# Kernel tuning notes

Measured on AMD Instinct MI355X. Metric: run time of the kernel, lower is better.

Reference implementation:

```python
import jax, jax.numpy as jnp
import numpy as np

S, B, D_IN, D_H, D_OUT = 32, 1024, 784, 1024, 10


def setup_inputs() -> dict:
    key = jax.random.key(0)
    ks = jax.random.split(key, 8)
    inp = {
        "x": jax.random.normal(ks[0], (B, D_IN), dtype=jnp.float32),
        # variational means / log-variances (init like the torch module)
        "wm0": jax.random.normal(ks[1], (D_IN, D_H), dtype=jnp.float32) * 0.1,
        "wv0": jnp.full((D_IN, D_H), -6.0, dtype=jnp.float32),
        "bm0": jnp.full((D_H,), 0.1, dtype=jnp.float32),
        "bv0": jnp.full((D_H,), -6.0, dtype=jnp.float32),
        "wm1": jax.random.normal(ks[2], (D_H, D_H), dtype=jnp.float32) * 0.1,
        "wv1": jnp.full((D_H, D_H), -6.0, dtype=jnp.float32),
        "bm1": jnp.full((D_H,), 0.1, dtype=jnp.float32),
        "bv1": jnp.full((D_H,), -6.0, dtype=jnp.float32),
        "wlm": jax.random.normal(ks[3], (D_H, D_OUT), dtype=jnp.float32) * 0.1,
        "wlv": jnp.full((D_H, D_OUT), -6.0, dtype=jnp.float32),
        "blm": jnp.full((D_OUT,), 0.1, dtype=jnp.float32),
        "blv": jnp.full((D_OUT,), -6.0, dtype=jnp.float32),
        # reparameterization noise (torch.randn in _predict), made explicit
        "we0": jax.random.normal(ks[4], (S, D_IN, D_H), dtype=jnp.float32),
        "be0": jax.random.normal(ks[5], (S, 1, D_H), dtype=jnp.float32),
        "we1": jax.random.normal(ks[6], (S, D_H, D_H), dtype=jnp.float32),
        "be1": jax.random.normal(ks[7], (S, 1, D_H), dtype=jnp.float32),
        "wel": jax.random.normal(jax.random.fold_in(key, 100), (S, D_H, D_OUT), dtype=jnp.float32),
        "bel": jax.random.normal(jax.random.fold_in(key, 101), (S, 1, D_OUT), dtype=jnp.float32),
    }
    return inp


def reference(x, wm0, wv0, bm0, bv0, wm1, wv1, bm1, bv1,
              wlm, wlv, blm, blv, we0, be0, we1, be1, wel, bel):
    n_samples = we0.shape[0]
    # activations: (S, B, D)
    act = jnp.broadcast_to(x[None], (n_samples,) + x.shape)
    for wm, wv, bm, bv, we, be in ((wm0, wv0, bm0, bv0, we0, be0),
                                   (wm1, wv1, bm1, bv1, we1, be1)):
        W = we * jnp.exp(0.5 * wv) + wm          # (S, in, out) sampled weights
        b = be * jnp.exp(0.5 * bv) + bm          # (S, 1, out) sampled biases
        act = jax.nn.relu(jnp.einsum('sbi,sio->sbo', act, W) + b)
    # last layer: torch does (act[...,None] * W[:,None]).sum(2) == batched matmul
    Wl = wel * jnp.exp(0.5 * wlv) + wlm
    bl = bel * jnp.exp(0.5 * blv) + blm
    logits = jnp.einsum('sbi,sio->sbo', act, Wl) + bl  # (S, B, D_OUT)
    return logits
```

## Files before the change

### kernel.cpp

```cpp
#include <hip/hip_runtime.h>

typedef unsigned short u16;
typedef __bf16 bf16x8 __attribute__((ext_vector_type(8)));
typedef float f32x4 __attribute__((ext_vector_type(4)));

__device__ __forceinline__ u16 f2bf(float f) {
  unsigned u = __builtin_bit_cast(unsigned, f);
  return (u16)((u + 0x7fffu + ((u >> 16) & 1u)) >> 16);
}

__device__ __forceinline__ void async_load16(const void* g, void* l) {
  __builtin_amdgcn_global_load_lds((const __attribute__((address_space(1))) void*)g,
                                   (__attribute__((address_space(3))) void*)l,
                                   16, 0, 0);
}

__global__ void pad_x_k(const float* __restrict__ x, u16* __restrict__ xbf) {
  int idx = blockIdx.x * 256 + threadIdx.x;
  int m = idx / 800, k = idx - m * 800;
  float v = (k < 784) ? x[m * 784 + k] : 0.f;
  xbf[idx] = f2bf(v);
}

__global__ void sample_w_k(const float* __restrict__ we,
                           const float* __restrict__ wm,
                           const float* __restrict__ wv,
                           u16* __restrict__ wt,
                           int K, int N, int Kp) {
  __shared__ float tile[32][33];
  int s = blockIdx.z;
  int k0 = blockIdx.x * 32, n0 = blockIdx.y * 32;
  int tx = threadIdx.x, ty = threadIdx.y;
  const float* we_s = we + (size_t)s * K * N;
#pragma unroll
  for (int r = ty; r < 32; r += 8) {
    int k = k0 + r, n = n0 + tx;
    float v = 0.f;
    if (k < K) {
      size_t idx = (size_t)k * N + n;
      v = fmaf(__expf(0.5f * wv[idx]), we_s[idx], wm[idx]);
    }
    tile[r][tx] = v;
  }
  __syncthreads();
  u16* wt_s = wt + (size_t)s * N * Kp;
#pragma unroll
  for (int r = ty; r < 32; r += 8) {
    int n = n0 + r, k = k0 + tx;
    wt_s[(size_t)n * Kp + k] = f2bf(tile[tx][r]);
  }
}

__global__ void sample_wl_k(const float* __restrict__ wel,
                            const float* __restrict__ wlm,
                            const float* __restrict__ wlv,
                            u16* __restrict__ wlt) {
  int idx = blockIdx.x * 256 + threadIdx.x;
  int k = idx & 1023;
  int n = (idx >> 10) & 15;
  int s = idx >> 14;
  float v = 0.f;
  if (n < 10) {
    size_t i2 = ((size_t)s * 1024 + k) * 10 + n;
    size_t iw = (size_t)k * 10 + n;
    v = fmaf(__expf(0.5f * wlv[iw]), wel[i2], wlm[iw]);
  }
  wlt[idx] = f2bf(v);
}

__global__ __launch_bounds__(256) void gemm_bt_relu(
    const u16* __restrict__ A, size_t strideAs, int ldA,
    const u16* __restrict__ Bt,
    u16* __restrict__ C,
    int K,
    const float* __restrict__ bm, const float* __restrict__ bv,
    const float* __restrict__ be, int s_off) {
  __shared__ __align__(16) u16 As[128 * 32];
  __shared__ __align__(16) u16 Bs[128 * 32];

  const int sc = blockIdx.z;
  const int sg = sc + s_off;
  const u16* A_s = A + (size_t)sc * strideAs;
  const u16* B_s = Bt + (size_t)sc * (size_t)1024 * K;
  u16* C_s = C + (size_t)sc * (size_t)1024 * 1024;

  const int m0 = blockIdx.y * 128;
  const int n0 = blockIdx.x * 128;
  const int t = threadIdx.x;
  const int w = t >> 6, l = t & 63;
  const int quad = l >> 4, lane16 = l & 15;
  const int wm_ = (w >> 1) * 64, wn_ = (w & 1) * 64;

  f32x4 acc[4][4];
#pragma unroll
  for (int i = 0; i < 4; ++i)
#pragma unroll
    for (int j = 0; j < 4; ++j) acc[i][j] = (f32x4){0.f, 0.f, 0.f, 0.f};

  for (int k0 = 0; k0 < K; k0 += 32) {
    __syncthreads();
#pragma unroll
    for (int i = 0; i < 2; ++i) {
      int p = w * 128 + i * 64 + l;
      const u16* srcA = A_s + (size_t)(m0 + (p >> 2)) * ldA + k0 + (p & 3) * 8;
      async_load16(srcA, &As[(size_t)(w * 128 + i * 64) * 8]);
      const u16* srcB = B_s + (size_t)(n0 + (p >> 2)) * K + k0 + (p & 3) * 8;
      async_load16(srcB, &Bs[(size_t)(w * 128 + i * 64) * 8]);
    }
    __syncthreads();

    bf16x8 af[4], bfr[4];
#pragma unroll
    for (int mi = 0; mi < 4; ++mi)
      af[mi] = *(const bf16x8*)&As[(wm_ + mi * 16 + lane16) * 32 + quad * 8];
#pragma unroll
    for (int ni = 0; ni < 4; ++ni)
      bfr[ni] = *(const bf16x8*)&Bs[(wn_ + ni * 16 + lane16) * 32 + quad * 8];
#pragma unroll
    for (int mi = 0; mi < 4; ++mi)
#pragma unroll
      for (int ni = 0; ni < 4; ++ni)
        acc[mi][ni] =
            __builtin_amdgcn_mfma_f32_16x16x32_bf16(af[mi], bfr[ni], acc[mi][ni], 0, 0, 0);
  }

#pragma unroll
  for (int ni = 0; ni < 4; ++ni) {
    int n = n0 + wn_ + ni * 16 + lane16;
    float bias = fmaf(__expf(0.5f * bv[n]), be[(size_t)sg * 1024 + n], bm[n]);
#pragma unroll
    for (int mi = 0; mi < 4; ++mi) {
#pragma unroll
      for (int r = 0; r < 4; ++r) {
        int m = m0 + wm_ + mi * 16 + quad * 4 + r;
        float v = acc[mi][ni][r] + bias;
        v = fmaxf(v, 0.f);
        C_s[(size_t)m * 1024 + n] = f2bf(v);
      }
    }
  }
}

__global__ __launch_bounds__(256) void gemm_last_k(
    const u16* __restrict__ act2, const u16* __restrict__ Wlt,
    float* __restrict__ out,
    const float* __restrict__ blm, const float* __restrict__ blv,
    const float* __restrict__ bel, int s_off) {
  const int sc = blockIdx.y;
  const int sg = sc + s_off;
  const int t = threadIdx.x;
  const int w = t >> 6, l = t & 63;
  const int quad = l >> 4, lane16 = l & 15;
  const int m0 = (blockIdx.x * 4 + w) * 16;

  const u16* A_s = act2 + (size_t)sc * 1024 * 1024;
  const u16* B_s = Wlt + (size_t)sc * 16 * 1024;

  f32x4 acc = (f32x4){0.f, 0.f, 0.f, 0.f};
#pragma unroll 4
  for (int k0 = 0; k0 < 1024; k0 += 32) {
    bf16x8 a = *(const bf16x8*)&A_s[(size_t)(m0 + lane16) * 1024 + k0 + quad * 8];
    bf16x8 b = *(const bf16x8*)&B_s[(size_t)lane16 * 1024 + k0 + quad * 8];
    acc = __builtin_amdgcn_mfma_f32_16x16x32_bf16(a, b, acc, 0, 0, 0);
  }
  int n = lane16;
  if (n < 10) {
    float bias = fmaf(__expf(0.5f * blv[n]), bel[sg * 10 + n], blm[n]);
#pragma unroll
    for (int r = 0; r < 4; ++r) {
      int m = m0 + quad * 4 + r;
      out[((size_t)sg * 1024 + m) * 10 + n] = acc[r] + bias;
    }
  }
}

extern "C" void kernel_launch(void* const* d_in, const int* in_sizes, int n_in,
                              void* d_out, int out_size, void* d_ws, size_t ws_size,
                              hipStream_t stream) {
  const float* x   = (const float*)d_in[0];
  const float* wm0 = (const float*)d_in[1];
  const float* wv0 = (const float*)d_in[2];
  const float* bm0 = (const float*)d_in[3];
  const float* bv0 = (const float*)d_in[4];
  const float* wm1 = (const float*)d_in[5];
  const float* wv1 = (const float*)d_in[6];
  const float* bm1 = (const float*)d_in[7];
  const float* bv1 = (const float*)d_in[8];
  const float* wlm = (const float*)d_in[9];
  const float* wlv = (const float*)d_in[10];
  const float* blm = (const float*)d_in[11];
  const float* blv = (const float*)d_in[12];
  const float* we0 = (const float*)d_in[13];
  const float* be0 = (const float*)d_in[14];
  const float* we1 = (const float*)d_in[15];
  const float* be1 = (const float*)d_in[16];
  const float* wel = (const float*)d_in[17];
  const float* bel = (const float*)d_in[18];
  float* out = (float*)d_out;

  const size_t sz_x    = (size_t)1024 * 800 * 2;
  const size_t sz_W0t  = (size_t)1024 * 800 * 2;
  const size_t sz_act  = (size_t)1024 * 1024 * 2;
  const size_t sz_Wlt  = (size_t)16 * 1024 * 2;
  const size_t per_s = sz_W0t + 3 * sz_act + sz_Wlt;

  int SC = 32;
  while (SC > 1 && sz_x + (size_t)SC * per_s + 4096 > ws_size) SC >>= 1;

  char* ws = (char*)d_ws;
  size_t off = 0;
  auto take = [&](size_t b) {
    char* p = ws + off;
    off = (off + b + 255) & ~(size_t)255;
    return p;
  };
  u16* xbf  = (u16*)take(sz_x);
  u16* W0t  = (u16*)take((size_t)SC * sz_W0t);
  u16* act1 = (u16*)take((size_t)SC * sz_act);
  u16* W1t  = (u16*)take((size_t)SC * sz_act);
  u16* act2 = (u16*)take((size_t)SC * sz_act);
  u16* Wlt  = (u16*)take((size_t)SC * sz_Wlt);

  pad_x_k<<<3200, 256, 0, stream>>>(x, xbf);

  for (int s0 = 0; s0 < 32; s0 += SC) {
    sample_w_k<<<dim3(25, 32, SC), dim3(32, 8), 0, stream>>>(
        we0 + (size_t)s0 * 784 * 1024, wm0, wv0, W0t, 784, 1024, 800);
    gemm_bt_relu<<<dim3(8, 8, SC), 256, 0, stream>>>(
        xbf, (size_t)0, 800, W0t, act1, 800, bm0, bv0, be0, s0);
    sample_w_k<<<dim3(32, 32, SC), dim3(32, 8), 0, stream>>>(
        we1 + (size_t)s0 * 1024 * 1024, wm1, wv1, W1t, 1024, 1024, 1024);
    gemm_bt_relu<<<dim3(8, 8, SC), 256, 0, stream>>>(
        act1, (size_t)1024 * 1024, 1024, W1t, act2, 1024, bm1, bv1, be1, s0);
    sample_wl_k<<<SC * 64, 256, 0, stream>>>(
        wel + (size_t)s0 * 1024 * 10, wlm, wlv, Wlt);
    gemm_last_k<<<dim3(16, SC), 256, 0, stream>>>(
        act2, Wlt, out, blm, blv, bel, s0);
  }
}
```

Baseline: 577.9 us.

## Reuse wm/exp(wv) across samples in weight sampling and remap blocks for XCD locality

The weight-sampling kernel is rewritten so each thread loads wm and computes exp(0.5*wv) once, then reuses them across several samples instead of reloading them per sample. It writes eight transposed bf16 values per 16-byte vector store, with no LDS transpose. All kernels switch to a 1D grid with a block-to-sample mapping that sends the same sample's blocks to the same XCD group (b&7), aiming for better L2 reuse of per-sample A/B tiles. The risk is that the transposed writes are strided by Kp per thread, and that mapping assumes round-robin XCD dispatch.

```diff
diff --git a/kernel.cpp b/kernel.cpp
--- a/kernel.cpp
+++ b/kernel.cpp
@@ -3,6 +3,7 @@
 typedef unsigned short u16;
 typedef __bf16 bf16x8 __attribute__((ext_vector_type(8)));
 typedef float f32x4 __attribute__((ext_vector_type(4)));
+typedef u16 u16x8 __attribute__((ext_vector_type(8)));
 
 __device__ __forceinline__ u16 f2bf(float f) {
   unsigned u = __builtin_bit_cast(unsigned, f);
@@ -22,32 +23,47 @@
   xbf[idx] = f2bf(v);
 }
 
-__global__ void sample_w_k(const float* __restrict__ we,
-                           const float* __restrict__ wm,
-                           const float* __restrict__ wv,
-                           u16* __restrict__ wt,
-                           int K, int N, int Kp) {
-  __shared__ float tile[32][33];
-  int s = blockIdx.z;
-  int k0 = blockIdx.x * 32, n0 = blockIdx.y * 32;
-  int tx = threadIdx.x, ty = threadIdx.y;
-  const float* we_s = we + (size_t)s * K * N;
-#pragma unroll
-  for (int r = ty; r < 32; r += 8) {
-    int k = k0 + r, n = n0 + tx;
-    float v = 0.f;
-    if (k < K) {
+__global__ __launch_bounds__(256) void sample_wt_k(
+    const float* __restrict__ we,
+    const float* __restrict__ wm,
+    const float* __restrict__ wv,
+    u16* __restrict__ wt,
+    int K, int N, int Kp, int SC) {
+  int b = blockIdx.x;
+  int g, inner, spg;
+  if (SC >= 8) { g = b & 7; inner = b >> 3; spg = SC >> 3; }
+  else         { g = b & (SC - 1); inner = b / SC; spg = 1; }
+  const int NB4 = N >> 8;
+  const int n4 = inner & (NB4 - 1);
+  const int kc = inner / NB4;
+  const int t = threadIdx.x;
+  const int n = (n4 << 8) + t;
+
+#pragma unroll 2
+  for (int ko = 0; ko < 8; ++ko) {
+    const int kbase = (kc << 6) + (ko << 3);
+    if (kbase >= Kp) break;
+    float wmr[8], sc[8];
+#pragma unroll
+    for (int j = 0; j < 8; ++j) {
+      int k = kbase + j;
+      bool ok = (k < K);
       size_t idx = (size_t)k * N + n;
-      v = fmaf(__expf(0.5f * wv[idx]), we_s[idx], wm[idx]);
-    }
-    tile[r][tx] = v;
-  }
-  __syncthreads();
-  u16* wt_s = wt + (size_t)s * N * Kp;
-#pragma unroll
-  for (int r = ty; r < 32; r += 8) {
-    int n = n0 + r, k = k0 + tx;
-    wt_s[(size_t)n * Kp + k] = f2bf(tile[tx][r]);
+      wmr[j] = ok ? wm[idx] : 0.f;
+      sc[j]  = ok ? __expf(0.5f * wv[idx]) : 0.f;
+    }
+    for (int si = 0; si < spg; ++si) {
+      const int s = g + (si << 3);
+      const float* we_s = we + (size_t)s * K * N;
+      u16x8 pk;
+#pragma unroll
+      for (int j = 0; j < 8; ++j) {
+        int k = kbase + j;
+        float v = (k < K) ? fmaf(sc[j], we_s[(size_t)k * N + n], wmr[j]) : 0.f;
+        pk[j] = f2bf(v);
+      }
+      *(u16x8*)(wt + ((size_t)s * N + n) * Kp + kbase) = pk;
+    }
   }
 }
 
@@ -74,18 +90,21 @@
     u16* __restrict__ C,
     int K,
     const float* __restrict__ bm, const float* __restrict__ bv,
-    const float* __restrict__ be, int s_off) {
+    const float* __restrict__ be, int s_off, int SC) {
   __shared__ __align__(16) u16 As[128 * 32];
   __shared__ __align__(16) u16 Bs[128 * 32];
 
-  const int sc = blockIdx.z;
+  const int b = blockIdx.x;
+  int sc, tile;
+  if (SC >= 8) { sc = (b & 7) + ((b >> 9) << 3); tile = (b >> 3) & 63; }
+  else         { sc = b >> 6; tile = b & 63; }
   const int sg = sc + s_off;
   const u16* A_s = A + (size_t)sc * strideAs;
   const u16* B_s = Bt + (size_t)sc * (size_t)1024 * K;
   u16* C_s = C + (size_t)sc * (size_t)1024 * 1024;
 
-  const int m0 = blockIdx.y * 128;
-  const int n0 = blockIdx.x * 128;
+  const int m0 = (tile >> 3) * 128;
+  const int n0 = (tile & 7) * 128;
   const int t = threadIdx.x;
   const int w = t >> 6, l = t & 63;
   const int quad = l >> 4, lane16 = l & 15;
@@ -145,13 +164,16 @@
     const u16* __restrict__ act2, const u16* __restrict__ Wlt,
     float* __restrict__ out,
     const float* __restrict__ blm, const float* __restrict__ blv,
-    const float* __restrict__ bel, int s_off) {
-  const int sc = blockIdx.y;
+    const float* __restrict__ bel, int s_off, int SC) {
+  const int b = blockIdx.x;
+  int sc, tile;
+  if (SC >= 8) { int g = b & 7, r = b >> 3; tile = r & 15; sc = g + ((r >> 4) << 3); }
+  else         { sc = b >> 4; tile = b & 15; }
   const int sg = sc + s_off;
   const int t = threadIdx.x;
   const int w = t >> 6, l = t & 63;
   const int quad = l >> 4, lane16 = l & 15;
-  const int m0 = (blockIdx.x * 4 + w) * 16;
+  const int m0 = (tile * 4 + w) * 16;
 
   const u16* A_s = act2 + (size_t)sc * 1024 * 1024;
   const u16* B_s = Wlt + (size_t)sc * 16 * 1024;
@@ -160,8 +182,8 @@
 #pragma unroll 4
   for (int k0 = 0; k0 < 1024; k0 += 32) {
     bf16x8 a = *(const bf16x8*)&A_s[(size_t)(m0 + lane16) * 1024 + k0 + quad * 8];
-    bf16x8 b = *(const bf16x8*)&B_s[(size_t)lane16 * 1024 + k0 + quad * 8];
-    acc = __builtin_amdgcn_mfma_f32_16x16x32_bf16(a, b, acc, 0, 0, 0);
+    bf16x8 bb = *(const bf16x8*)&B_s[(size_t)lane16 * 1024 + k0 + quad * 8];
+    acc = __builtin_amdgcn_mfma_f32_16x16x32_bf16(a, bb, acc, 0, 0, 0);
   }
   int n = lane16;
   if (n < 10) {
@@ -209,9 +231,9 @@
 
   char* ws = (char*)d_ws;
   size_t off = 0;
-  auto take = [&](size_t b) {
+  auto take = [&](size_t bsz) {
     char* p = ws + off;
-    off = (off + b + 255) & ~(size_t)255;
+    off = (off + bsz + 255) & ~(size_t)255;
     return p;
   };
   u16* xbf  = (u16*)take(sz_x);
@@ -223,18 +245,22 @@
 
   pad_x_k<<<3200, 256, 0, stream>>>(x, xbf);
 
+  const int gdim_s = (SC >= 8) ? 8 : SC;
+  const int kc0 = (800 + 63) / 64;
+  const int kc1 = 1024 / 64;
+
   for (int s0 = 0; s0 < 32; s0 += SC) {
-    sample_w_k<<<dim3(25, 32, SC), dim3(32, 8), 0, stream>>>(
-        we0 + (size_t)s0 * 784 * 1024, wm0, wv0, W0t, 784, 1024, 800);
-    gemm_bt_relu<<<dim3(8, 8, SC), 256, 0, stream>>>(
-        xbf, (size_t)0, 800, W0t, act1, 800, bm0, bv0, be0, s0);
-    sample_w_k<<<dim3(32, 32, SC), dim3(32, 8), 0, stream>>>(
-        we1 + (size_t)s0 * 1024 * 1024, wm1, wv1, W1t, 1024, 1024, 1024);
-    gemm_bt_relu<<<dim3(8, 8, SC), 256, 0, stream>>>(
-        act1, (size_t)1024 * 1024, 1024, W1t, act2, 1024, bm1, bv1, be1, s0);
+    sample_wt_k<<<gdim_s * 4 * kc0, 256, 0, stream>>>(
+        we0 + (size_t)s0 * 784 * 1024, wm0, wv0, W0t, 784, 1024, 800, SC);
+    gemm_bt_relu<<<64 * SC, 256, 0, stream>>>(
+        xbf, (size_t)0, 800, W0t, act1, 800, bm0, bv0, be0, s0, SC);
+    sample_wt_k<<<gdim_s * 4 * kc1, 256, 0, stream>>>(
+        we1 + (size_t)s0 * 1024 * 1024, wm1, wv1, W1t, 1024, 1024, 1024, SC);
+    gemm_bt_relu<<<64 * SC, 256, 0, stream>>>(
+        act1, (size_t)1024 * 1024, 1024, W1t, act2, 1024, bm1, bv1, be1, s0, SC);
     sample_wl_k<<<SC * 64, 256, 0, stream>>>(
         wel + (size_t)s0 * 1024 * 10, wlm, wlv, Wlt);
-    gemm_last_k<<<dim3(16, SC), 256, 0, stream>>>(
-        act2, Wlt, out, blm, blv, bel, s0);
-  }
-}
+    gemm_last_k<<<16 * SC, 256, 0, stream>>>(
+        act2, Wlt, out, blm, blv, bel, s0, SC);
+  }
+}
```

Result: slower. 937.9 us (+62.3%).
